# Performance work log

Measured on AMD Instinct MI355X. Metric: run time of the kernel, lower is better.

The kernel has to match this reference:

```python
import jax, jax.numpy as jnp
import numpy as np

VOCAB, T, CLASSES = 30000, 256, 2
B, E, H = 128, 300, 256


def setup_inputs() -> dict:
    key = jax.random.key(0)
    ks = jax.random.split(key, 16)
    s = lambda k, sh, sc=0.02: jax.random.normal(k, sh, dtype=jnp.float32) * sc
    return {
        "tokens": jax.random.randint(ks[0], (B, T), 0, VOCAB, dtype=jnp.int32),
        "mask": jax.random.randint(ks[1], (B, T), 0, 2) > 0,
        "emb": s(ks[2], (VOCAB, E)),
        "Wi": s(ks[3], (E, 4 * H)),
        "Wh": s(ks[4], (H, 4 * H)),
        "b_lstm": jnp.zeros((4 * H,), jnp.float32),
        "Wq": s(ks[5], (H, H)), "bq": jnp.zeros((H,), jnp.float32),
        "Wk": s(ks[6], (H, H)), "bk": jnp.zeros((H,), jnp.float32),
        "Wv": s(ks[7], (H, H)), "bv": jnp.zeros((H,), jnp.float32),
        "Wo": s(ks[8], (H, H)), "bo": jnp.zeros((H,), jnp.float32),
        "W1": s(ks[9], (T * H, 100)), "b1": jnp.zeros((100,), jnp.float32),
        "W2": s(ks[10], (100, CLASSES)), "b2": jnp.zeros((CLASSES,), jnp.float32),
    }


def _forward(tokens, mask, emb, Wi, Wh, b_lstm, Wq, bq, Wk, bk, Wv, bv, Wo, bo, W1, b1, W2, b2):
    x = emb[tokens]  # (B, T, E)
    bsz = x.shape[0]
    # Pre-project inputs once (equivalent math, fewer per-step FLOPs)
    xW = jnp.einsum('bte,eg->btg', x, Wi) + b_lstm  # (B, T, 4H)

    def step(carry, xt):
        c, h = carry
        y = xt + h @ Wh  # (B, 4H)
        i, f, g, o = jnp.split(y, 4, axis=-1)  # flax OptimizedLSTMCell gate order
        i, f, o = jax.nn.sigmoid(i), jax.nn.sigmoid(f), jax.nn.sigmoid(o)
        g = jnp.tanh(g)
        c = f * c + i * g
        h = o * jnp.tanh(c)
        return (c, h), h

    c0 = jnp.zeros((bsz, H), x.dtype)
    h0 = jnp.zeros((bsz, H), x.dtype)
    _, hs = jax.lax.scan(step, (c0, h0), jnp.swapaxes(xW, 0, 1))
    hs = jnp.swapaxes(hs, 0, 1)  # (B, T, H)

    # single-head self-attention (flax SelfAttention(1))
    q = (hs @ Wq + bq) / jnp.sqrt(jnp.asarray(H, hs.dtype))
    k = hs @ Wk + bk
    v = hs @ Wv + bv
    scores = jnp.einsum('bqd,bkd->bqk', q, k)  # (B, T, T)
    # mask repeated 'b v -> b 1 v max_length': masks query rows, broadcast over keys
    big_neg = jnp.finfo(scores.dtype).min
    scores = jnp.where(mask[:, :, None], scores, big_neg)
    w = jax.nn.softmax(scores, axis=-1)
    attn = jnp.einsum('bqk,bkd->bqd', w, v) @ Wo + bo  # (B, T, H)

    flat = attn.reshape(bsz, -1)  # (B, T*H)
    h1 = jax.nn.relu(flat @ W1 + b1)
    logits = h1 @ W2 + b2
    return jax.nn.softmax(logits, axis=-1)


def reference(tokens, mask, emb, Wi, Wh, b_lstm, Wq, bq, Wk, bk, Wv, bv, Wo, bo, W1, b1, W2, b2):
    return _forward(tokens, mask, emb, Wi, Wh, b_lstm, Wq, bq, Wk, bk, Wv, bv, Wo, bo, W1, b1, W2, b2)
```

## Files before the change

### kernel.cpp

```cpp
#include <hip/hip_runtime.h>
#include <stdint.h>

#define B_   128
#define T_   256
#define H_   256
#define E_   300
#define G4_  1024

typedef __attribute__((ext_vector_type(8))) short bf16x8s;
typedef __attribute__((ext_vector_type(4))) float f32x4;

__device__ __forceinline__ short f2bf(float f) {
    unsigned u = __builtin_bit_cast(unsigned, f);
    unsigned r = (u + 0x7fffu + ((u >> 16) & 1u)) >> 16;
    return (short)r;
}
__device__ __forceinline__ float bf2f(short s) {
    unsigned u = (unsigned)(unsigned short)s;
    return __builtin_bit_cast(float, u << 16);
}
__device__ __forceinline__ float sigm(float x) { return 1.f / (1.f + __expf(-x)); }
__device__ __forceinline__ float ftanh(float x) {
    float e = __expf(-2.f * x);
    return (1.f - e) / (1.f + e);
}

__global__ void k_detect(const unsigned char* __restrict__ m8, int* __restrict__ flag) {
    int i = blockIdx.x * 256 + threadIdx.x;
    if ((i & 3) != 0 && m8[i] != 0) atomicOr(flag, 1);
}

__global__ void k_prep(const void* __restrict__ mask, const int* __restrict__ tokens,
                       const int* __restrict__ flag, float* __restrict__ maskf,
                       int* __restrict__ rowtok) {
    int i = blockIdx.x * 256 + threadIdx.x;
    int isbyte = *flag;
    int mv = isbyte ? (int)((const unsigned char*)mask)[i] : ((const int*)mask)[i];
    maskf[i] = mv ? 1.f : 0.f;
    int b = i >> 8, t = i & 255;
    rowtok[t * B_ + b] = tokens[i];
}

__global__ void k_bpack(const float* __restrict__ W, short* __restrict__ out,
                        int N, int KS, int KREAL) {
    int frag = blockIdx.x;
    int nt = frag / KS, ks = frag - nt * KS;
    int l = threadIdx.x;
    int col = nt * 16 + (l & 15);
    int k0 = ks * 32 + (l >> 4) * 8;
    short tmp[8];
#pragma unroll
    for (int i = 0; i < 8; ++i) {
        int k = k0 + i;
        tmp[i] = (k < KREAL) ? f2bf(W[(size_t)k * N + col]) : (short)0;
    }
    int4 v;
    __builtin_memcpy(&v, tmp, 16);
    ((int4*)out)[(size_t)frag * 64 + l] = v;
}

__global__ void k_packqkv(const float* __restrict__ Wq, const float* __restrict__ Wk,
                          const float* __restrict__ Wv, short* __restrict__ out) {
    int frag = blockIdx.x;
    int nt = frag >> 3, ks = frag & 7;
    int l = threadIdx.x;
    int col = (nt & 15) * 16 + (l & 15);
    int k0 = ks * 32 + (l >> 4) * 8;
    const float* W = nt < 16 ? Wq : (nt < 32 ? Wk : Wv);
    float sc = nt < 16 ? 0.0625f : 1.f;
    short tmp[8];
#pragma unroll
    for (int i = 0; i < 8; ++i) tmp[i] = f2bf(W[(size_t)(k0 + i) * 256 + col] * sc);
    int4 v;
    __builtin_memcpy(&v, tmp, 16);
    ((int4*)out)[(size_t)frag * 64 + l] = v;
}

__global__ void k_bias3(const float* __restrict__ bq, const float* __restrict__ bk,
                        const float* __restrict__ bv, float* __restrict__ bqkv) {
    int i = threadIdx.x;
    float v;
    if (i < 256) v = bq[i] * 0.0625f;
    else if (i < 512) v = bk[i - 256];
    else v = bv[i - 512];
    bqkv[i] = v;
}

template<bool GATHER, bool ABF16, int OUTMODE, int KS>
__global__ __launch_bounds__(512) void k_gemm_mfma(
    const void* __restrict__ Av, const short* __restrict__ Bp,
    const float* __restrict__ bias, void* __restrict__ Cv,
    void* __restrict__ C2, void* __restrict__ C3,
    int N, int KREAL, const int* __restrict__ rowidx)
{
    constexpr int KP = KS * 32;
    constexpr int LDA = KP + 8;
    __shared__ __align__(16) short As[128 * LDA];
    const int tid = threadIdx.x;
    const int l = tid & 63, w = tid >> 6;
    const int cl = l & 15, rowq = l >> 4;
    const int m0 = blockIdx.x * 128;

    for (int e = tid; e < 128 * KP; e += 512) {
        int r = e / KP, k = e - r * KP;
        int row = m0 + r;
        int arow = GATHER ? rowidx[row] : row;
        short sv = 0;
        if (k < KREAL) {
            if constexpr (ABF16) sv = ((const short*)Av)[(size_t)arow * KREAL + k];
            else                 sv = f2bf(((const float*)Av)[(size_t)arow * KREAL + k]);
        }
        As[r * LDA + k] = sv;
    }
    __syncthreads();

    bf16x8s a[KS];
#pragma unroll
    for (int ks = 0; ks < KS; ++ks)
        a[ks] = *(const bf16x8s*)&As[(w * 16 + cl) * LDA + ks * 32 + rowq * 8];

    const int nchunks = N >> 8;
    for (int ch = 0; ch < nchunks; ++ch) {
#pragma unroll
        for (int ntl = 0; ntl < 16; ++ntl) {
            const int nt = ch * 16 + ntl;
            const float bv = bias[nt * 16 + cl];
            f32x4 y = {bv, bv, bv, bv};
#pragma unroll
            for (int ks = 0; ks < KS; ++ks) {
                bf16x8s bf = *(const bf16x8s*)&Bp[((size_t)(nt * KS + ks) * 64 + l) * 8];
                y = __builtin_amdgcn_mfma_f32_16x16x32_bf16(a[ks], bf, y, 0, 0, 0);
            }
            if constexpr (OUTMODE == 2) {
                const int t  = m0 >> 7;
                const int wl = (nt >> 1) & 7, pp = nt & 1, gg = nt >> 4;
                const size_t fi = ((((size_t)t * 8 + w) * 8 + wl) * 2 + pp) * 4 + gg;
                short4 o;
                o.x = f2bf(y[0]); o.y = f2bf(y[1]); o.z = f2bf(y[2]); o.w = f2bf(y[3]);
                *(short4*)&((short*)Cv)[fi * 256 + (size_t)l * 4] = o;
            } else if constexpr (OUTMODE == 3) {
                const int gg = nt >> 4;
                if (gg < 2) {
                    short* dst = gg ? (short*)C2 : (short*)Cv;
#pragma unroll
                    for (int r = 0; r < 4; ++r) {
                        size_t row = (size_t)m0 + w * 16 + rowq * 4 + r;
                        dst[row * 256 + (nt & 15) * 16 + cl] = f2bf(y[r]);
                    }
                } else {
                    const int bidx = m0 >> 8;
                    const int t0 = (m0 & 255) + w * 16 + rowq * 4;
                    const int d = (nt & 15) * 16 + cl;
                    short4 o;
                    o.x = f2bf(y[0]); o.y = f2bf(y[1]); o.z = f2bf(y[2]); o.w = f2bf(y[3]);
                    *(short4*)&((short*)C3)[((size_t)bidx * 256 + d) * 256 + t0] = o;
                }
            } else {
#pragma unroll
                for (int r = 0; r < 4; ++r) {
                    size_t idx = (size_t)(m0 + w * 16 + rowq * 4 + r) * N + nt * 16 + cl;
                    ((float*)Cv)[idx] = y[r];
                }
            }
        }
    }
}

#define LDA_H 264

__global__ __launch_bounds__(512, 2) void lstm_mfma(
    const short* __restrict__ xwp, const short* __restrict__ whp,
    short* __restrict__ hs)
{
    __shared__ __align__(16) short whc[128 * 64 * 8];
    __shared__ __align__(16) short hb[2][16 * LDA_H];
    const int tid = threadIdx.x;
    const int l = tid & 63;
    const int w = tid >> 6;
    const int cl = l & 15;
    const int rowq = l >> 4;
    const int bb = blockIdx.x;
    const int bbase = bb * 16;

    for (int e = tid; e < 128 * 64; e += 512) {
        int frag = e >> 6, q = e & 63;
        int nt = frag >> 1, ks = frag & 1;
        ((int4*)whc)[e] = ((const int4*)whp)[(nt * 8 + ks) * 64 + q];
    }
    for (int e = tid; e < 2 * 16 * LDA_H; e += 512) ((short*)hb)[e] = 0;

    bf16x8s wreg[2][4][4];
#pragma unroll
    for (int p = 0; p < 2; ++p)
#pragma unroll
        for (int g = 0; g < 4; ++g)
#pragma unroll
            for (int kr = 0; kr < 4; ++kr) {
                const int nt = g * 16 + w * 2 + p;
                wreg[p][g][kr] = *(const bf16x8s*)&whp[((size_t)(nt * 8 + 2 + kr) * 64 + l) * 8];
            }

    float creg[2][4];
#pragma unroll
    for (int p = 0; p < 2; ++p)
#pragma unroll
        for (int r = 0; r < 4; ++r) creg[p][r] = 0.f;

    const short* xbase = xwp + ((size_t)bb * 8 + w) * 2 * 4 * 256 + (size_t)l * 4;
    const size_t tstride = (size_t)8 * 8 * 2 * 4 * 256;

    auto ld_xw = [&](int t, short4 (&dst)[2][4]) {
        const short* p0 = xbase + (size_t)t * tstride;
#pragma unroll
        for (int p = 0; p < 2; ++p)
#pragma unroll
            for (int g = 0; g < 4; ++g)
                dst[p][g] = *(const short4*)&p0[(p * 4 + g) * 256];
    };

    short4 xwA[2][4], xwB[2][4];
    ld_xw(0, xwA);
    __syncthreads();

    auto step = [&](int t, short4 (&cur)[2][4], short4 (&nxt)[2][4]) {
        ld_xw(t + 1, nxt);

        const short* hbr = hb[t & 1];
        short* hbw = hb[(t + 1) & 1];
        bf16x8s a[8];
#pragma unroll
        for (int ks = 0; ks < 8; ++ks)
            a[ks] = *(const bf16x8s*)&hbr[cl * LDA_H + ks * 32 + rowq * 8];

        f32x4 y[2][4];
#pragma unroll
        for (int p = 0; p < 2; ++p)
#pragma unroll
            for (int g = 0; g < 4; ++g) {
                y[p][g][0] = bf2f(cur[p][g].x);
                y[p][g][1] = bf2f(cur[p][g].y);
                y[p][g][2] = bf2f(cur[p][g].z);
                y[p][g][3] = bf2f(cur[p][g].w);
            }

#pragma unroll
        for (int p = 0; p < 2; ++p) {
#pragma unroll
            for (int g = 0; g < 4; ++g) {
                const int nt = g * 16 + w * 2 + p;
                const size_t sb = ((size_t)nt * 8 * 64 + l) * 8;
                bf16x8s s6 = *(const bf16x8s*)&whp[sb + 6 * 64 * 8];
                bf16x8s s7 = *(const bf16x8s*)&whp[sb + 7 * 64 * 8];
                bf16x8s c0 = *(const bf16x8s*)&whc[((nt * 2 + 0) * 64 + l) * 8];
                bf16x8s c1 = *(const bf16x8s*)&whc[((nt * 2 + 1) * 64 + l) * 8];
                y[p][g] = __builtin_amdgcn_mfma_f32_16x16x32_bf16(a[2], wreg[p][g][0], y[p][g], 0, 0, 0);
                y[p][g] = __builtin_amdgcn_mfma_f32_16x16x32_bf16(a[3], wreg[p][g][1], y[p][g], 0, 0, 0);
                y[p][g] = __builtin_amdgcn_mfma_f32_16x16x32_bf16(a[4], wreg[p][g][2], y[p][g], 0, 0, 0);
                y[p][g] = __builtin_amdgcn_mfma_f32_16x16x32_bf16(a[5], wreg[p][g][3], y[p][g], 0, 0, 0);
                y[p][g] = __builtin_amdgcn_mfma_f32_16x16x32_bf16(a[0], c0, y[p][g], 0, 0, 0);
                y[p][g] = __builtin_amdgcn_mfma_f32_16x16x32_bf16(a[1], c1, y[p][g], 0, 0, 0);
                y[p][g] = __builtin_amdgcn_mfma_f32_16x16x32_bf16(a[6], s6, y[p][g], 0, 0, 0);
                y[p][g] = __builtin_amdgcn_mfma_f32_16x16x32_bf16(a[7], s7, y[p][g], 0, 0, 0);
            }
        }

#pragma unroll
        for (int p = 0; p < 2; ++p) {
            const int j = w * 32 + p * 16 + cl;
#pragma unroll
            for (int r = 0; r < 4; ++r) {
                float iv = sigm(y[p][0][r]);
                float fv = sigm(y[p][1][r]);
                float gv = ftanh(y[p][2][r]);
                float ov = sigm(y[p][3][r]);
                float c = fmaf(fv, creg[p][r], iv * gv);
                creg[p][r] = c;
                float hv = ov * ftanh(c);
                short hvb = f2bf(hv);
                int b = rowq * 4 + r;
                hbw[b * LDA_H + j] = hvb;
                hs[((size_t)(bbase + b) * T_ + t) * H_ + j] = hvb;
            }
        }
        __syncthreads();
    };

    for (int t = 0; t < T_; t += 2) {
        step(t,     xwA, xwB);
        step(t + 1, xwB, xwA);
    }
}

__global__ __launch_bounds__(256) void k_attn_mfma(
    const short* __restrict__ qb, const short* __restrict__ kb,
    const short* __restrict__ vt, const float* __restrict__ maskf,
    float* __restrict__ o)
{
    __shared__ __align__(16) short P_lds[4][16 * 40];
    const int tid = threadIdx.x;
    const int l = tid & 63, w = tid >> 6;
    const int cl = l & 15, qr = l >> 4;
    const int b = blockIdx.y;
    const int q0 = blockIdx.x * 64 + w * 16;
    const size_t bb = (size_t)b * 256;

    bf16x8s qf[8];
    const short* qrow = qb + (bb + q0 + cl) * 256;
#pragma unroll
    for (int ks = 0; ks < 8; ++ks)
        qf[ks] = *(const bf16x8s*)&qrow[ks * 32 + qr * 8];

    float4 mr4 = *(const float4*)&maskf[bb + q0 + qr * 4];
    float msk[4] = {mr4.x, mr4.y, mr4.z, mr4.w};

    float m[4] = {-1e30f, -1e30f, -1e30f, -1e30f};
    float ls[4] = {0.f, 0.f, 0.f, 0.f};
    f32x4 acc[16];
#pragma unroll
    for (int nt = 0; nt < 16; ++nt) acc[nt] = {0.f, 0.f, 0.f, 0.f};

    for (int kt2 = 0; kt2 < 8; ++kt2) {
        const short* krow0 = kb + (bb + kt2 * 32 + cl) * 256;
        f32x4 s0 = {0.f, 0.f, 0.f, 0.f}, s1 = {0.f, 0.f, 0.f, 0.f};
#pragma unroll
        for (int ks = 0; ks < 8; ++ks) {
            bf16x8s k0f = *(const bf16x8s*)&krow0[ks * 32 + qr * 8];
            bf16x8s k1f = *(const bf16x8s*)&krow0[16 * 256 + ks * 32 + qr * 8];
            s0 = __builtin_amdgcn_mfma_f32_16x16x32_bf16(qf[ks], k0f, s0, 0, 0, 0);
            s1 = __builtin_amdgcn_mfma_f32_16x16x32_bf16(qf[ks], k1f, s1, 0, 0, 0);
        }

#pragma unroll
        for (int r = 0; r < 4; ++r) {
            float a0 = (msk[r] != 0.f) ? s0[r] : 0.f;
            float a1 = (msk[r] != 0.f) ? s1[r] : 0.f;
            float t = fmaxf(a0, a1);
            t = fmaxf(t, __shfl_xor(t, 1));
            t = fmaxf(t, __shfl_xor(t, 2));
            t = fmaxf(t, __shfl_xor(t, 4));
            t = fmaxf(t, __shfl_xor(t, 8));
            float mnew = fmaxf(m[r], t);
            float rsc = __expf(m[r] - mnew);
            m[r] = mnew;
            float p0 = __expf(a0 - mnew);
            float p1 = __expf(a1 - mnew);
            float ps = p0 + p1;
            ps += __shfl_xor(ps, 1);
            ps += __shfl_xor(ps, 2);
            ps += __shfl_xor(ps, 4);
            ps += __shfl_xor(ps, 8);
            ls[r] = ls[r] * rsc + ps;
#pragma unroll
            for (int nt = 0; nt < 16; ++nt) acc[nt][r] *= rsc;
            P_lds[w][(qr * 4 + r) * 40 + cl] = f2bf(p0);
            P_lds[w][(qr * 4 + r) * 40 + 16 + cl] = f2bf(p1);
        }

        bf16x8s pa = *(const bf16x8s*)&P_lds[w][cl * 40 + qr * 8];
        const short* vrow = vt + (bb + cl) * 256 + kt2 * 32 + qr * 8;
#pragma unroll
        for (int nt = 0; nt < 16; ++nt) {
            bf16x8s vf = *(const bf16x8s*)&vrow[(size_t)nt * 16 * 256];
            acc[nt] = __builtin_amdgcn_mfma_f32_16x16x32_bf16(pa, vf, acc[nt], 0, 0, 0);
        }
    }

    float inv[4];
#pragma unroll
    for (int r = 0; r < 4; ++r) inv[r] = 1.f / ls[r];
#pragma unroll
    for (int nt = 0; nt < 16; ++nt)
#pragma unroll
        for (int r = 0; r < 4; ++r)
            o[(bb + q0 + qr * 4 + r) * 256 + nt * 16 + cl] = acc[nt][r] * inv[r];
}

__global__ __launch_bounds__(256) void k_fc1(
    const float* __restrict__ flat, const float* __restrict__ W1, float* __restrict__ part)
{
    __shared__ __align__(16) float Wt[100][260];
    __shared__ __align__(16) float fs[2][256];
    const int kc = blockIdx.x, tid = threadIdx.x;
    for (int e = tid; e < 25600; e += 256) {
        int k = e / 100, j = e - k * 100;
        Wt[j][k] = W1[(size_t)(kc * 256 + k) * 100 + j];
    }
    __syncthreads();
    const int bh = tid / 100, j = tid - bh * 100;
    for (int bb = 0; bb < 64; ++bb) {
        for (int e = tid; e < 512; e += 256) {
            int bi = e >> 8, k = e & 255;
            fs[bi][k] = flat[(size_t)(bb * 2 + bi) * 65536 + kc * 256 + k];
        }
        __syncthreads();
        if (bh < 2) {
            float acc = 0.f;
#pragma unroll 16
            for (int k = 0; k < 256; k += 4) {
                float4 fv = *(const float4*)&fs[bh][k];
                float4 wv = *(const float4*)&Wt[j][k];
                acc = fmaf(fv.x, wv.x, fmaf(fv.y, wv.y, fmaf(fv.z, wv.z, fmaf(fv.w, wv.w, acc))));
            }
            part[(size_t)kc * 12800 + (bb * 2 + bh) * 100 + j] = acc;
        }
        __syncthreads();
    }
}

__global__ __launch_bounds__(128) void k_head(
    const float* __restrict__ part, const float* __restrict__ b1,
    const float* __restrict__ W2, const float* __restrict__ b2, float* __restrict__ out)
{
    __shared__ float h1s[100];
    __shared__ float ls[2];
    const int b = blockIdx.x, tid = threadIdx.x;
    if (tid < 100) {
        float s = 0.f;
        for (int kc = 0; kc < 256; ++kc) s += part[(size_t)kc * 12800 + b * 100 + tid];
        s += b1[tid];
        h1s[tid] = fmaxf(s, 0.f);
    }
    __syncthreads();
    if (tid < 2) {
        float lg = b2[tid];
        for (int j = 0; j < 100; ++j) lg = fmaf(h1s[j], W2[j * 2 + tid], lg);
        ls[tid] = lg;
    }
    __syncthreads();
    if (tid == 0) {
        float mm = fmaxf(ls[0], ls[1]);
        float e0 = __expf(ls[0] - mm), e1 = __expf(ls[1] - mm);
        float inv = 1.f / (e0 + e1);
        out[b * 2 + 0] = e0 * inv;
        out[b * 2 + 1] = e1 * inv;
    }
}

extern "C" void kernel_launch(void* const* d_in, const int* in_sizes, int n_in,
                              void* d_out, int out_size, void* d_ws, size_t ws_size,
                              hipStream_t stream) {
    (void)in_sizes; (void)n_in; (void)out_size; (void)ws_size;
    const int*   tokens = (const int*)  d_in[0];
    const void*  mask   =               d_in[1];
    const float* emb    = (const float*)d_in[2];
    const float* Wi     = (const float*)d_in[3];
    const float* Wh     = (const float*)d_in[4];
    const float* b_lstm = (const float*)d_in[5];
    const float* Wq     = (const float*)d_in[6];
    const float* bq     = (const float*)d_in[7];
    const float* Wk     = (const float*)d_in[8];
    const float* bk     = (const float*)d_in[9];
    const float* Wv     = (const float*)d_in[10];
    const float* bv     = (const float*)d_in[11];
    const float* Wo     = (const float*)d_in[12];
    const float* bo     = (const float*)d_in[13];
    const float* W1     = (const float*)d_in[14];
    const float* b1     = (const float*)d_in[15];
    const float* W2     = (const float*)d_in[16];
    const float* b2     = (const float*)d_in[17];
    float* out = (float*)d_out;

    float* ws = (float*)d_ws;
    float* reg0  = ws;
    short* xwp   = (short*)reg0;
    float* hsb   = reg0 + 33554432;
    short* hsb16 = (short*)hsb;
    float* maskf = hsb + 8388608;
    int*   rowtok= (int*)(maskf + 32768);
    int*   flag  = rowtok + 32768;
    short* whp   = (short*)((((uintptr_t)(flag + 1)) + 255) & ~(uintptr_t)255);
    short* wip   = whp + 262144;
    short* wqkvp = wip + 327680;
    short* wop   = wqkvp + 196608;
    float* bqkv  = (float*)(wop + 65536);
    short* qb16 = (short*)reg0;
    short* kb16 = (short*)(reg0 + 4194304);
    short* vt16 = (short*)(reg0 + 8388608);
    float* proj = reg0 + 12582912;
    float* part = reg0 + 20971520;
    float* attnf = hsb;

    hipMemsetAsync(flag, 0, sizeof(int), stream);
    k_detect<<<128, 256, 0, stream>>>((const unsigned char*)mask, flag);
    k_prep<<<128, 256, 0, stream>>>(mask, tokens, flag, maskf, rowtok);

    k_bpack<<<512, 64, 0, stream>>>(Wh, whp, 1024, 8, 256);
    k_bpack<<<640, 64, 0, stream>>>(Wi, wip, 1024, 10, 300);
    k_packqkv<<<384, 64, 0, stream>>>(Wq, Wk, Wv, wqkvp);
    k_bias3<<<1, 768, 0, stream>>>(bq, bk, bv, bqkv);
    k_bpack<<<128, 64, 0, stream>>>(Wo, wop, 256, 8, 256);

    k_gemm_mfma<true, false, 2, 10><<<256, 512, 0, stream>>>(
        emb, wip, b_lstm, xwp, nullptr, nullptr, 1024, 300, rowtok);

    lstm_mfma<<<8, 512, 0, stream>>>(xwp, whp, hsb16);

    k_gemm_mfma<false, true, 3, 8><<<256, 512, 0, stream>>>(
        hsb16, wqkvp, bqkv, qb16, kb16, vt16, 768, 256, nullptr);

    k_attn_mfma<<<dim3(4, 128), 256, 0, stream>>>(qb16, kb16, vt16, maskf, attnf);

    k_gemm_mfma<false, false, 0, 8><<<256, 512, 0, stream>>>(
        attnf, wop, bo, proj, nullptr, nullptr, 256, 256, nullptr);

    k_fc1<<<256, 256, 0, stream>>>(proj, W1, part);
    k_head<<<128, 128, 0, stream>>>(part, b1, W2, b2, out);
}
```

Measured before the change: 1.710 ms.

## Stage B tiles in LDS and compute two M-subtiles per wave in GEMM

The MFMA GEMM kernel now runs 256 threads per block, with each wave computing two 16-row subtiles so every B fragment feeds two MFMAs. B fragments for four N-tiles at a time are cooperatively copied into shared memory rather than read directly from global memory by each wave. The aim is to halve global B traffic per block and raise arithmetic intensity. In exchange it adds block-wide barriers per group of N-tiles, uses more registers for A fragments, and halves the wave count used for the A-tile load.

```diff
diff --git a/kernel.cpp b/kernel.cpp
--- a/kernel.cpp
+++ b/kernel.cpp
@@ -87,7 +87,7 @@
 }
 
 template<bool GATHER, bool ABF16, int OUTMODE, int KS>
-__global__ __launch_bounds__(512) void k_gemm_mfma(
+__global__ __launch_bounds__(256) void k_gemm_mfma(
     const void* __restrict__ Av, const short* __restrict__ Bp,
     const float* __restrict__ bias, void* __restrict__ Cv,
     void* __restrict__ C2, void* __restrict__ C3,
@@ -96,12 +96,13 @@
     constexpr int KP = KS * 32;
     constexpr int LDA = KP + 8;
     __shared__ __align__(16) short As[128 * LDA];
+    __shared__ __align__(16) short Bs[4 * KS * 512];
     const int tid = threadIdx.x;
     const int l = tid & 63, w = tid >> 6;
     const int cl = l & 15, rowq = l >> 4;
     const int m0 = blockIdx.x * 128;
 
-    for (int e = tid; e < 128 * KP; e += 512) {
+    for (int e = tid; e < 128 * KP; e += 256) {
         int r = e / KP, k = e - r * KP;
         int row = m0 + r;
         int arow = GATHER ? rowidx[row] : row;
@@ -114,52 +115,71 @@
     }
     __syncthreads();
 
-    bf16x8s a[KS];
-#pragma unroll
-    for (int ks = 0; ks < KS; ++ks)
-        a[ks] = *(const bf16x8s*)&As[(w * 16 + cl) * LDA + ks * 32 + rowq * 8];
+    bf16x8s a[2][KS];
+#pragma unroll
+    for (int s = 0; s < 2; ++s)
+#pragma unroll
+        for (int ks = 0; ks < KS; ++ks)
+            a[s][ks] = *(const bf16x8s*)&As[((w * 2 + s) * 16 + cl) * LDA + ks * 32 + rowq * 8];
 
     const int nchunks = N >> 8;
     for (int ch = 0; ch < nchunks; ++ch) {
-#pragma unroll
-        for (int ntl = 0; ntl < 16; ++ntl) {
-            const int nt = ch * 16 + ntl;
-            const float bv = bias[nt * 16 + cl];
-            f32x4 y = {bv, bv, bv, bv};
-#pragma unroll
-            for (int ks = 0; ks < KS; ++ks) {
-                bf16x8s bf = *(const bf16x8s*)&Bp[((size_t)(nt * KS + ks) * 64 + l) * 8];
-                y = __builtin_amdgcn_mfma_f32_16x16x32_bf16(a[ks], bf, y, 0, 0, 0);
-            }
-            if constexpr (OUTMODE == 2) {
-                const int t  = m0 >> 7;
-                const int wl = (nt >> 1) & 7, pp = nt & 1, gg = nt >> 4;
-                const size_t fi = ((((size_t)t * 8 + w) * 8 + wl) * 2 + pp) * 4 + gg;
-                short4 o;
-                o.x = f2bf(y[0]); o.y = f2bf(y[1]); o.z = f2bf(y[2]); o.w = f2bf(y[3]);
-                *(short4*)&((short*)Cv)[fi * 256 + (size_t)l * 4] = o;
-            } else if constexpr (OUTMODE == 3) {
-                const int gg = nt >> 4;
-                if (gg < 2) {
-                    short* dst = gg ? (short*)C2 : (short*)Cv;
-#pragma unroll
-                    for (int r = 0; r < 4; ++r) {
-                        size_t row = (size_t)m0 + w * 16 + rowq * 4 + r;
-                        dst[row * 256 + (nt & 15) * 16 + cl] = f2bf(y[r]);
+        for (int qt = 0; qt < 4; ++qt) {
+            const int nt0 = ch * 16 + qt * 4;
+            __syncthreads();
+            for (int e = tid; e < 4 * KS * 64; e += 256)
+                ((int4*)Bs)[e] = ((const int4*)Bp)[(size_t)nt0 * KS * 64 + e];
+            __syncthreads();
+#pragma unroll
+            for (int q2 = 0; q2 < 4; ++q2) {
+                const int nt = nt0 + q2;
+                const float bv = bias[nt * 16 + cl];
+                f32x4 y0 = {bv, bv, bv, bv}, y1 = {bv, bv, bv, bv};
+#pragma unroll
+                for (int ks = 0; ks < KS; ++ks) {
+                    bf16x8s bf = *(const bf16x8s*)&Bs[((q2 * KS + ks) * 64 + l) * 8];
+                    y0 = __builtin_amdgcn_mfma_f32_16x16x32_bf16(a[0][ks], bf, y0, 0, 0, 0);
+                    y1 = __builtin_amdgcn_mfma_f32_16x16x32_bf16(a[1][ks], bf, y1, 0, 0, 0);
+                }
+                if constexpr (OUTMODE == 2) {
+                    const int t  = m0 >> 7;
+                    const int wl = (nt >> 1) & 7, pp = nt & 1, gg = nt >> 4;
+                    const size_t fb = (((size_t)t * 8 + w * 2) * 8 + wl) * 2;
+                    short4 o0, o1;
+                    o0.x = f2bf(y0[0]); o0.y = f2bf(y0[1]); o0.z = f2bf(y0[2]); o0.w = f2bf(y0[3]);
+                    o1.x = f2bf(y1[0]); o1.y = f2bf(y1[1]); o1.z = f2bf(y1[2]); o1.w = f2bf(y1[3]);
+                    *(short4*)&((short*)Cv)[((fb + pp) * 4 + gg) * 256 + (size_t)l * 4] = o0;
+                    *(short4*)&((short*)Cv)[((fb + 16 + pp) * 4 + gg) * 256 + (size_t)l * 4] = o1;
+                } else if constexpr (OUTMODE == 3) {
+                    const int gg = nt >> 4;
+                    if (gg < 2) {
+                        short* dst = gg ? (short*)C2 : (short*)Cv;
+#pragma unroll
+                        for (int r = 0; r < 4; ++r) {
+                            size_t r0 = (size_t)m0 + (w * 2 + 0) * 16 + rowq * 4 + r;
+                            size_t r1 = (size_t)m0 + (w * 2 + 1) * 16 + rowq * 4 + r;
+                            dst[r0 * 256 + (nt & 15) * 16 + cl] = f2bf(y0[r]);
+                            dst[r1 * 256 + (nt & 15) * 16 + cl] = f2bf(y1[r]);
+                        }
+                    } else {
+                        const int bidx = m0 >> 8;
+                        const int d = (nt & 15) * 16 + cl;
+                        const int t00 = (m0 & 255) + (w * 2 + 0) * 16 + rowq * 4;
+                        const int t01 = (m0 & 255) + (w * 2 + 1) * 16 + rowq * 4;
+                        short4 o0, o1;
+                        o0.x = f2bf(y0[0]); o0.y = f2bf(y0[1]); o0.z = f2bf(y0[2]); o0.w = f2bf(y0[3]);
+                        o1.x = f2bf(y1[0]); o1.y = f2bf(y1[1]); o1.z = f2bf(y1[2]); o1.w = f2bf(y1[3]);
+                        *(short4*)&((short*)C3)[((size_t)bidx * 256 + d) * 256 + t00] = o0;
+                        *(short4*)&((short*)C3)[((size_t)bidx * 256 + d) * 256 + t01] = o1;
                     }
                 } else {
-                    const int bidx = m0 >> 8;
-                    const int t0 = (m0 & 255) + w * 16 + rowq * 4;
-                    const int d = (nt & 15) * 16 + cl;
-                    short4 o;
-                    o.x = f2bf(y[0]); o.y = f2bf(y[1]); o.z = f2bf(y[2]); o.w = f2bf(y[3]);
-                    *(short4*)&((short*)C3)[((size_t)bidx * 256 + d) * 256 + t0] = o;
-                }
-            } else {
-#pragma unroll
-                for (int r = 0; r < 4; ++r) {
-                    size_t idx = (size_t)(m0 + w * 16 + rowq * 4 + r) * N + nt * 16 + cl;
-                    ((float*)Cv)[idx] = y[r];
+#pragma unroll
+                    for (int r = 0; r < 4; ++r) {
+                        size_t r0 = (size_t)m0 + (w * 2 + 0) * 16 + rowq * 4 + r;
+                        size_t r1 = (size_t)m0 + (w * 2 + 1) * 16 + rowq * 4 + r;
+                        ((float*)Cv)[r0 * N + nt * 16 + cl] = y0[r];
+                        ((float*)Cv)[r1 * N + nt * 16 + cl] = y1[r];
+                    }
                 }
             }
         }
@@ -490,17 +510,17 @@
     k_bias3<<<1, 768, 0, stream>>>(bq, bk, bv, bqkv);
     k_bpack<<<128, 64, 0, stream>>>(Wo, wop, 256, 8, 256);
 
-    k_gemm_mfma<true, false, 2, 10><<<256, 512, 0, stream>>>(
+    k_gemm_mfma<true, false, 2, 10><<<256, 256, 0, stream>>>(
         emb, wip, b_lstm, xwp, nullptr, nullptr, 1024, 300, rowtok);
 
     lstm_mfma<<<8, 512, 0, stream>>>(xwp, whp, hsb16);
 
-    k_gemm_mfma<false, true, 3, 8><<<256, 512, 0, stream>>>(
+    k_gemm_mfma<false, true, 3, 8><<<256, 256, 0, stream>>>(
         hsb16, wqkvp, bqkv, qb16, kb16, vt16, 768, 256, nullptr);
 
     k_attn_mfma<<<dim3(4, 128), 256, 0, stream>>>(qb16, kb16, vt16, maskf, attnf);
 
-    k_gemm_mfma<false, false, 0, 8><<<256, 512, 0, stream>>>(
+    k_gemm_mfma<false, false, 0, 8><<<256, 256, 0, stream>>>(
         attnf, wop, bo, proj, nullptr, nullptr, 256, 256, nullptr);
 
     k_fc1<<<256, 256, 0, stream>>>(proj, W1, part);
```

Result: slower. 1.761 ms (+3.0%).

## Overlap input-projection GEMM with LSTM recurrence via per-timestep flags; store proj in bf16

Applied to the files above, without the earlier changes.

Fuses the embedding-gather input-projection GEMM and the LSTM recurrence into one cooperative launch. Eight blocks run the recurrence while the remaining blocks compute xW per timestep and publish it through release/acquire flags, so the sequential LSTM can start before the whole projection finishes. Separately, the Wo projection output is written as bf16 and converted back in fc1, halving that intermediate's traffic at some precision cost. The design depends on all blocks being co-resident and on spin-waiting being safe.

```diff
diff --git a/kernel.cpp b/kernel.cpp
--- a/kernel.cpp
+++ b/kernel.cpp
@@ -131,14 +131,7 @@
                 bf16x8s bf = *(const bf16x8s*)&Bp[((size_t)(nt * KS + ks) * 64 + l) * 8];
                 y = __builtin_amdgcn_mfma_f32_16x16x32_bf16(a[ks], bf, y, 0, 0, 0);
             }
-            if constexpr (OUTMODE == 2) {
-                const int t  = m0 >> 7;
-                const int wl = (nt >> 1) & 7, pp = nt & 1, gg = nt >> 4;
-                const size_t fi = ((((size_t)t * 8 + w) * 8 + wl) * 2 + pp) * 4 + gg;
-                short4 o;
-                o.x = f2bf(y[0]); o.y = f2bf(y[1]); o.z = f2bf(y[2]); o.w = f2bf(y[3]);
-                *(short4*)&((short*)Cv)[fi * 256 + (size_t)l * 4] = o;
-            } else if constexpr (OUTMODE == 3) {
+            if constexpr (OUTMODE == 3) {
                 const int gg = nt >> 4;
                 if (gg < 2) {
                     short* dst = gg ? (short*)C2 : (short*)Cv;
@@ -155,6 +148,12 @@
                     o.x = f2bf(y[0]); o.y = f2bf(y[1]); o.z = f2bf(y[2]); o.w = f2bf(y[3]);
                     *(short4*)&((short*)C3)[((size_t)bidx * 256 + d) * 256 + t0] = o;
                 }
+            } else if constexpr (OUTMODE == 1) {
+#pragma unroll
+                for (int r = 0; r < 4; ++r) {
+                    size_t idx = (size_t)(m0 + w * 16 + rowq * 4 + r) * N + nt * 16 + cl;
+                    ((short*)Cv)[idx] = f2bf(y[r]);
+                }
             } else {
 #pragma unroll
                 for (int r = 0; r < 4; ++r) {
@@ -168,18 +167,68 @@
 
 #define LDA_H 264
 
-__global__ __launch_bounds__(512, 2) void lstm_mfma(
-    const short* __restrict__ xwp, const short* __restrict__ whp,
-    short* __restrict__ hs)
+__global__ __launch_bounds__(512, 2) void k_lstm_gather(
+    const float* __restrict__ emb, const short* __restrict__ wip,
+    const float* __restrict__ b_lstm, const int* __restrict__ rowtok,
+    short* __restrict__ xwp, const short* __restrict__ whp,
+    short* __restrict__ hs, int* __restrict__ flags)
 {
-    __shared__ __align__(16) short whc[128 * 64 * 8];
-    __shared__ __align__(16) short hb[2][16 * LDA_H];
+    __shared__ __align__(16) short lds_u[73984];
     const int tid = threadIdx.x;
     const int l = tid & 63;
     const int w = tid >> 6;
     const int cl = l & 15;
     const int rowq = l >> 4;
-    const int bb = blockIdx.x;
+    const int blk = blockIdx.x;
+
+    if (blk >= 8) {
+        constexpr int KP = 320, LDA = 328;
+        short* As = lds_u;
+        for (int u = blk - 8; u < 256; u += 248) {
+            const int m0 = u * 128;
+            __syncthreads();
+            for (int e = tid; e < 128 * KP; e += 512) {
+                int r = e / KP, k = e - r * KP;
+                int arow = rowtok[m0 + r];
+                short sv = 0;
+                if (k < E_) sv = f2bf(emb[(size_t)arow * E_ + k]);
+                As[r * LDA + k] = sv;
+            }
+            __syncthreads();
+            bf16x8s a[10];
+#pragma unroll
+            for (int ks = 0; ks < 10; ++ks)
+                a[ks] = *(const bf16x8s*)&As[(w * 16 + cl) * LDA + ks * 32 + rowq * 8];
+
+            for (int ch = 0; ch < 4; ++ch) {
+#pragma unroll
+                for (int ntl = 0; ntl < 16; ++ntl) {
+                    const int nt = ch * 16 + ntl;
+                    const float bv = b_lstm[nt * 16 + cl];
+                    f32x4 y = {bv, bv, bv, bv};
+#pragma unroll
+                    for (int ks = 0; ks < 10; ++ks) {
+                        bf16x8s bf = *(const bf16x8s*)&wip[((size_t)(nt * 10 + ks) * 64 + l) * 8];
+                        y = __builtin_amdgcn_mfma_f32_16x16x32_bf16(a[ks], bf, y, 0, 0, 0);
+                    }
+                    const int wl = (nt >> 1) & 7, pp = nt & 1, gg = nt >> 4;
+                    const size_t fi = ((((size_t)u * 8 + w) * 8 + wl) * 2 + pp) * 4 + gg;
+                    short4 o;
+                    o.x = f2bf(y[0]); o.y = f2bf(y[1]); o.z = f2bf(y[2]); o.w = f2bf(y[3]);
+                    *(short4*)&xwp[fi * 256 + (size_t)l * 4] = o;
+                }
+            }
+            __threadfence();
+            __syncthreads();
+            if (tid == 0)
+                __hip_atomic_store(flags + u, 1, __ATOMIC_RELEASE, __HIP_MEMORY_SCOPE_AGENT);
+        }
+        return;
+    }
+
+    short* whc = lds_u;
+    short* hbp = lds_u + 65536;
+    const int bb = blk;
     const int bbase = bb * 16;
 
     for (int e = tid; e < 128 * 64; e += 512) {
@@ -187,7 +236,7 @@
         int nt = frag >> 1, ks = frag & 1;
         ((int4*)whc)[e] = ((const int4*)whp)[(nt * 8 + ks) * 64 + q];
     }
-    for (int e = tid; e < 2 * 16 * LDA_H; e += 512) ((short*)hb)[e] = 0;
+    for (int e = tid; e < 2 * 16 * LDA_H; e += 512) hbp[e] = 0;
 
     bf16x8s wreg[2][4][4];
 #pragma unroll
@@ -209,6 +258,10 @@
     const short* xbase = xwp + ((size_t)bb * 8 + w) * 2 * 4 * 256 + (size_t)l * 4;
     const size_t tstride = (size_t)8 * 8 * 2 * 4 * 256;
 
+    auto wait_t = [&](int t) {
+        if (t < 256)
+            while (__hip_atomic_load(flags + t, __ATOMIC_ACQUIRE, __HIP_MEMORY_SCOPE_AGENT) == 0) {}
+    };
     auto ld_xw = [&](int t, short4 (&dst)[2][4]) {
         const short* p0 = xbase + (size_t)t * tstride;
 #pragma unroll
@@ -219,14 +272,16 @@
     };
 
     short4 xwA[2][4], xwB[2][4];
+    wait_t(0);
     ld_xw(0, xwA);
     __syncthreads();
 
     auto step = [&](int t, short4 (&cur)[2][4], short4 (&nxt)[2][4]) {
+        wait_t(t + 1);
         ld_xw(t + 1, nxt);
 
-        const short* hbr = hb[t & 1];
-        short* hbw = hb[(t + 1) & 1];
+        const short* hbr = hbp + (t & 1) * (16 * LDA_H);
+        short* hbw = hbp + ((t + 1) & 1) * (16 * LDA_H);
         bf16x8s a[8];
 #pragma unroll
         for (int ks = 0; ks < 8; ++ks)
@@ -376,7 +431,7 @@
 }
 
 __global__ __launch_bounds__(256) void k_fc1(
-    const float* __restrict__ flat, const float* __restrict__ W1, float* __restrict__ part)
+    const short* __restrict__ flat, const float* __restrict__ W1, float* __restrict__ part)
 {
     __shared__ __align__(16) float Wt[100][260];
     __shared__ __align__(16) float fs[2][256];
@@ -390,7 +445,7 @@
     for (int bb = 0; bb < 64; ++bb) {
         for (int e = tid; e < 512; e += 256) {
             int bi = e >> 8, k = e & 255;
-            fs[bi][k] = flat[(size_t)(bb * 2 + bi) * 65536 + kc * 256 + k];
+            fs[bi][k] = bf2f(flat[(size_t)(bb * 2 + bi) * 65536 + kc * 256 + k]);
         }
         __syncthreads();
         if (bh < 2) {
@@ -473,14 +528,16 @@
     short* wqkvp = wip + 327680;
     short* wop   = wqkvp + 196608;
     float* bqkv  = (float*)(wop + 65536);
+    int*   flags = (int*)(bqkv + 768);
     short* qb16 = (short*)reg0;
     short* kb16 = (short*)(reg0 + 4194304);
     short* vt16 = (short*)(reg0 + 8388608);
-    float* proj = reg0 + 12582912;
+    short* projb= (short*)(reg0 + 12582912);
     float* part = reg0 + 20971520;
     float* attnf = hsb;
 
     hipMemsetAsync(flag, 0, sizeof(int), stream);
+    hipMemsetAsync(flags, 0, 256 * sizeof(int), stream);
     k_detect<<<128, 256, 0, stream>>>((const unsigned char*)mask, flag);
     k_prep<<<128, 256, 0, stream>>>(mask, tokens, flag, maskf, rowtok);
 
@@ -490,19 +547,22 @@
     k_bias3<<<1, 768, 0, stream>>>(bq, bk, bv, bqkv);
     k_bpack<<<128, 64, 0, stream>>>(Wo, wop, 256, 8, 256);
 
-    k_gemm_mfma<true, false, 2, 10><<<256, 512, 0, stream>>>(
-        emb, wip, b_lstm, xwp, nullptr, nullptr, 1024, 300, rowtok);
-
-    lstm_mfma<<<8, 512, 0, stream>>>(xwp, whp, hsb16);
+    {
+        const float* a0 = emb; const short* a1 = wip; const float* a2 = b_lstm;
+        const int* a3 = rowtok; short* a4 = xwp; const short* a5 = whp;
+        short* a6 = hsb16; int* a7 = flags;
+        void* kargs[] = {&a0, &a1, &a2, &a3, &a4, &a5, &a6, &a7};
+        hipLaunchCooperativeKernel((void*)k_lstm_gather, dim3(256), dim3(512), kargs, 0, stream);
+    }
 
     k_gemm_mfma<false, true, 3, 8><<<256, 512, 0, stream>>>(
         hsb16, wqkvp, bqkv, qb16, kb16, vt16, 768, 256, nullptr);
 
     k_attn_mfma<<<dim3(4, 128), 256, 0, stream>>>(qb16, kb16, vt16, maskf, attnf);
 
-    k_gemm_mfma<false, false, 0, 8><<<256, 512, 0, stream>>>(
-        attnf, wop, bo, proj, nullptr, nullptr, 256, 256, nullptr);
-
-    k_fc1<<<256, 256, 0, stream>>>(proj, W1, part);
+    k_gemm_mfma<false, false, 1, 8><<<256, 512, 0, stream>>>(
+        attnf, wop, bo, projb, nullptr, nullptr, 256, 256, nullptr);
+
+    k_fc1<<<256, 256, 0, stream>>>(projb, W1, part);
     k_head<<<128, 128, 0, stream>>>(part, b1, W2, b2, out);
 }
```

Result: slower. 2.563 ms (+49.9%).
